# Kernel tuning notes

Measured on AMD Instinct MI355X. Metric: run time of the kernel, lower is better.

The kernel has to match this reference:

```python
import jax, jax.numpy as jnp
import numpy as np

B, S = 16, 4096
E_ENC, E_DEC, H = 1024, 1024, 512


def setup_inputs() -> dict:
    key = jax.random.key(0)
    ks = jax.random.split(key, 8)
    sc_e = 1.0 / np.sqrt(E_ENC)
    sc_d = 1.0 / np.sqrt(E_DEC)
    sc_h = 1.0 / np.sqrt(H)
    return {
        "encoder_hiddens": jax.random.normal(ks[0], (B, S, E_ENC), jnp.float32),
        "decoder_hidden": jax.random.normal(ks[1], (B, E_DEC), jnp.float32),
        "We": jax.random.uniform(ks[2], (E_ENC, H), jnp.float32, -sc_e, sc_e),
        "be": jax.random.uniform(ks[3], (H,), jnp.float32, -sc_e, sc_e),
        "Wd": jax.random.uniform(ks[4], (E_DEC, H), jnp.float32, -sc_d, sc_d),
        "bd": jax.random.uniform(ks[5], (H,), jnp.float32, -sc_d, sc_d),
        "Wo": jax.random.uniform(ks[6], (H, 1), jnp.float32, -sc_h, sc_h),
        "bo": jax.random.uniform(ks[7], (1,), jnp.float32, -sc_h, sc_h),
    }


def reference(encoder_hiddens, decoder_hidden, We, be, Wd, bd, Wo, bo):
    # Additive (Bahdanau) attention.
    # enc_proj: [B,S,H]; dec_proj: [B,1,H] broadcast over sequence.
    enc_proj = jnp.einsum("bse,eh->bsh", encoder_hiddens, We) + be
    dec_proj = jnp.einsum("bd,dh->bh", decoder_hidden, Wd) + bd
    e = jnp.tanh(enc_proj + dec_proj[:, None, :])          # [B,S,H]
    scores = jnp.einsum("bsh,h->bs", e, Wo[:, 0]) + bo[0]  # [B,S]
    attn = jax.nn.softmax(scores, axis=-1)                 # [B,S]
    context = jnp.einsum("bs,bse->be", attn, encoder_hiddens)  # [B,E_ENC]
    return context
```

## Files before the change

kernel.cpp:

```cpp
#include <hip/hip_runtime.h>
#include <hip/hip_bf16.h>
#include <math.h>

#define B_ 16
#define S_ 4096
#define E_ 1024
#define H_ 512

typedef short bf16x8 __attribute__((ext_vector_type(8)));
typedef unsigned short u16x8 __attribute__((ext_vector_type(8)));
typedef float f32x4 __attribute__((ext_vector_type(4)));

__device__ inline unsigned short f2bf(float x) {
    __hip_bfloat16 h = __float2bfloat16(x);
    return *(unsigned short*)&h;
}

__global__ __launch_bounds__(256) void we_transpose_kernel(
    const float* __restrict__ We, unsigned short* __restrict__ WeT) {
    __shared__ float sT[64][65];
    int k0 = (blockIdx.x >> 3) * 64;
    int n0 = (blockIdx.x & 7) * 64;
    int t = threadIdx.x;
#pragma unroll
    for (int p = 0; p < 16; ++p) {
        int idx = p * 256 + t;
        int k = idx >> 6, n = idx & 63;
        sT[n][k] = We[(size_t)(k0 + k) * H_ + n0 + n];
    }
    __syncthreads();
#pragma unroll
    for (int p = 0; p < 16; ++p) {
        int idx = p * 256 + t;
        int n = idx >> 6, k = idx & 63;
        WeT[(size_t)(n0 + n) * E_ + k0 + k] = f2bf(sT[n][k]);
    }
}

__global__ __launch_bounds__(256) void dp_kernel(const float* __restrict__ dec,
                                                 const float* __restrict__ Wd,
                                                 const float* __restrict__ bd,
                                                 const float* __restrict__ be,
                                                 float* __restrict__ dp) {
    int b = blockIdx.x >> 3;
    int hc = blockIdx.x & 7;
    int t = threadIdx.x;
    int h = hc * 64 + (t & 63);
    int ec = t >> 6;
    const float* dr = dec + b * E_ + ec * 256;
    const float* wp = Wd + (size_t)(ec * 256) * H_ + h;
    float acc = 0.f;
#pragma unroll 8
    for (int e = 0; e < 256; ++e) acc = fmaf(dr[e], wp[(size_t)e * H_], acc);
    __shared__ float red[4][64];
    red[ec][t & 63] = acc;
    __syncthreads();
    if (t < 64) {
        int hh = hc * 64 + t;
        dp[b * H_ + hh] = red[0][t] + red[1][t] + red[2][t] + red[3][t] + bd[hh] + be[hh];
    }
}

#define BM 128
#define BN 128
#define BK 32
#define LDA 40

__global__ __launch_bounds__(256) void scores_mfma_kernel(
    const float* __restrict__ enc, const unsigned short* __restrict__ WeT,
    const float* __restrict__ Wo, const float* __restrict__ dp,
    float* __restrict__ parts) {
    __shared__ unsigned short sA[BM * LDA];
    __shared__ unsigned short sB[BN * LDA];
    __shared__ float sRed[2][BM];

    int tid = threadIdx.x;
    int nt = blockIdx.x & 3;
    int mt = blockIdx.x >> 2;
    int m0 = mt * BM;
    int n0 = nt * BN;
    int b = m0 >> 12;
    int wave = tid >> 6, lane = tid & 63;
    int wm = wave & 1, wn = wave >> 1;
    int quad = lane >> 4, l16 = lane & 15;

    f32x4 acc[4][4];
#pragma unroll
    for (int i = 0; i < 4; ++i)
#pragma unroll
        for (int j = 0; j < 4; ++j) acc[i][j] = (f32x4)0.f;

    int am = tid >> 3;
    int ac = (tid & 7) * 4;
    const float* encP = enc + (size_t)(m0 + am) * E_ + ac;
    unsigned short* sAp = sA + am * LDA + ac;
    int bn = tid >> 1, bh = tid & 1;
    const unsigned short* wtP = WeT + (size_t)(n0 + bn) * E_ + bh * 16;
    unsigned short* sBp = sB + bn * LDA + bh * 16;

    int aBase = (wm * 64 + l16) * LDA + quad * 8;
    int bBase = (wn * 64 + l16) * LDA + quad * 8;

    for (int k0 = 0; k0 < E_; k0 += BK) {
        __syncthreads();
#pragma unroll
        for (int p = 0; p < 4; ++p) {
            float4 v = *(const float4*)(encP + (size_t)p * 32 * E_ + k0);
            ushort4 u;
            u.x = f2bf(v.x); u.y = f2bf(v.y); u.z = f2bf(v.z); u.w = f2bf(v.w);
            *(ushort4*)(sAp + p * 32 * LDA) = u;
        }
        u16x8 w0 = *(const u16x8*)(wtP + k0);
        u16x8 w1 = *(const u16x8*)(wtP + k0 + 8);
        *(u16x8*)(sBp) = w0;
        *(u16x8*)(sBp + 8) = w1;
        __syncthreads();

        bf16x8 aR[4], bR[4];
#pragma unroll
        for (int i = 0; i < 4; ++i) aR[i] = *(const bf16x8*)(sA + aBase + i * 16 * LDA);
#pragma unroll
        for (int j = 0; j < 4; ++j) bR[j] = *(const bf16x8*)(sB + bBase + j * 16 * LDA);
#pragma unroll
        for (int i = 0; i < 4; ++i)
#pragma unroll
            for (int j = 0; j < 4; ++j)
                acc[i][j] = __builtin_amdgcn_mfma_f32_16x16x32_bf16(aR[i], bR[j], acc[i][j], 0, 0, 0);
    }

    float dpv[4], wov[4];
#pragma unroll
    for (int j = 0; j < 4; ++j) {
        int h = n0 + wn * 64 + j * 16 + l16;
        dpv[j] = dp[b * H_ + h];
        wov[j] = Wo[h];
    }
    float part[4][4];
#pragma unroll
    for (int i = 0; i < 4; ++i)
#pragma unroll
        for (int r = 0; r < 4; ++r) {
            float s = 0.f;
#pragma unroll
            for (int j = 0; j < 4; ++j) {
                float x = acc[i][j][r] + dpv[j];
                float e = __expf(2.f * x);
                s += (1.f - 2.f / (e + 1.f)) * wov[j];
            }
            part[i][r] = s;
        }
#pragma unroll
    for (int i = 0; i < 4; ++i)
#pragma unroll
        for (int r = 0; r < 4; ++r) {
            float s = part[i][r];
            s += __shfl_xor(s, 1, 64);
            s += __shfl_xor(s, 2, 64);
            s += __shfl_xor(s, 4, 64);
            s += __shfl_xor(s, 8, 64);
            part[i][r] = s;
        }
    if (l16 == 0) {
#pragma unroll
        for (int i = 0; i < 4; ++i)
#pragma unroll
            for (int r = 0; r < 4; ++r)
                sRed[wn][wm * 64 + i * 16 + quad * 4 + r] = part[i][r];
    }
    __syncthreads();
    if (tid < BM) {
        float sc = sRed[0][tid] + sRed[1][tid];
        int s = (m0 & (S_ - 1)) + tid;
        parts[(size_t)(nt * B_ + b) * S_ + s] = sc;
    }
}

__global__ __launch_bounds__(256) void softmax_kernel(float* __restrict__ parts) {
    int b = blockIdx.x;
    const float* p0 = parts + (size_t)(0 * B_ + b) * S_;
    const float* p1 = parts + (size_t)(1 * B_ + b) * S_;
    const float* p2 = parts + (size_t)(2 * B_ + b) * S_;
    const float* p3 = parts + (size_t)(3 * B_ + b) * S_;
    float* row = parts + (size_t)b * S_;
    int tid = threadIdx.x;
    float v[16];
    float m = -1e30f;
#pragma unroll
    for (int i = 0; i < 16; ++i) {
        int idx = i * 256 + tid;
        v[i] = p0[idx] + p1[idx] + p2[idx] + p3[idx];
        m = fmaxf(m, v[i]);
    }
    for (int off = 32; off; off >>= 1) m = fmaxf(m, __shfl_xor(m, off, 64));
    __shared__ float redm[4];
    __shared__ float reds[4];
    if ((tid & 63) == 0) redm[tid >> 6] = m;
    __syncthreads();
    m = fmaxf(fmaxf(redm[0], redm[1]), fmaxf(redm[2], redm[3]));
    float s = 0.f;
#pragma unroll
    for (int i = 0; i < 16; ++i) {
        v[i] = __expf(v[i] - m);
        s += v[i];
    }
    for (int off = 32; off; off >>= 1) s += __shfl_xor(s, off, 64);
    if ((tid & 63) == 0) reds[tid >> 6] = s;
    __syncthreads();
    s = reds[0] + reds[1] + reds[2] + reds[3];
    float inv = 1.f / s;
#pragma unroll
    for (int i = 0; i < 16; ++i) row[i * 256 + tid] = v[i] * inv;
}

__global__ __launch_bounds__(256) void zero_kernel(float* __restrict__ out) {
    out[blockIdx.x * 256 + threadIdx.x] = 0.f;
}

__global__ __launch_bounds__(256) void ctx_kernel(const float* __restrict__ enc,
                                                  const float* __restrict__ attn,
                                                  float* __restrict__ out) {
    int b = blockIdx.x >> 5;
    int s0 = (blockIdx.x & 31) * 128;
    int tid = threadIdx.x;
    __shared__ float w[128];
    if (tid < 128) w[tid] = attn[(size_t)b * S_ + s0 + tid];
    __syncthreads();
    const float* base = enc + ((size_t)b * S_ + s0) * E_ + tid * 4;
    float4 acc = make_float4(0.f, 0.f, 0.f, 0.f);
    for (int s = 0; s < 128; ++s) {
        float4 v = *(const float4*)(base + (size_t)s * E_);
        float ws = w[s];
        acc.x = fmaf(ws, v.x, acc.x);
        acc.y = fmaf(ws, v.y, acc.y);
        acc.z = fmaf(ws, v.z, acc.z);
        acc.w = fmaf(ws, v.w, acc.w);
    }
    float* o = out + b * E_ + tid * 4;
    atomicAdd(o + 0, acc.x);
    atomicAdd(o + 1, acc.y);
    atomicAdd(o + 2, acc.z);
    atomicAdd(o + 3, acc.w);
}

extern "C" void kernel_launch(void* const* d_in, const int* in_sizes, int n_in,
                              void* d_out, int out_size, void* d_ws, size_t ws_size,
                              hipStream_t stream) {
    const float* enc = (const float*)d_in[0];
    const float* dec = (const float*)d_in[1];
    const float* We  = (const float*)d_in[2];
    const float* be  = (const float*)d_in[3];
    const float* Wd  = (const float*)d_in[4];
    const float* bd  = (const float*)d_in[5];
    const float* Wo  = (const float*)d_in[6];
    float* out = (float*)d_out;

    char* w = (char*)d_ws;
    unsigned short* WeT = (unsigned short*)w;
    float* dp = (float*)(w + (1 << 20));
    float* parts = (float*)(w + (1 << 20) + 32768);
    float* attn = parts;

    we_transpose_kernel<<<128, 256, 0, stream>>>(We, WeT);
    dp_kernel<<<B_ * 8, 256, 0, stream>>>(dec, Wd, bd, be, dp);
    scores_mfma_kernel<<<(B_ * S_ / BM) * (H_ / BN), 256, 0, stream>>>(enc, WeT, Wo, dp, parts);
    softmax_kernel<<<B_, 256, 0, stream>>>(parts);
    zero_kernel<<<(B_ * E_) / 256, 256, 0, stream>>>(out);
    ctx_kernel<<<B_ * 32, 256, 0, stream>>>(enc, attn, out);
}
```

Measured before the change: 539.6 us.

## Pre-convert encoder to bf16, use direct-to-LDS loads and deterministic context reduction

```diff
diff --git a/kernel.cpp b/kernel.cpp
--- a/kernel.cpp
+++ b/kernel.cpp
@@ -7,6 +7,11 @@
 #define E_ 1024
 #define H_ 512
 
+#define BM 128
+#define BN 128
+#define BK 64
+#define NCHUNK (E_ / BK)
+
 typedef short bf16x8 __attribute__((ext_vector_type(8)));
 typedef unsigned short u16x8 __attribute__((ext_vector_type(8)));
 typedef float f32x4 __attribute__((ext_vector_type(4)));
@@ -15,74 +20,95 @@
     __hip_bfloat16 h = __float2bfloat16(x);
     return *(unsigned short*)&h;
 }
-
-__global__ __launch_bounds__(256) void we_transpose_kernel(
-    const float* __restrict__ We, unsigned short* __restrict__ WeT) {
-    __shared__ float sT[64][65];
-    int k0 = (blockIdx.x >> 3) * 64;
-    int n0 = (blockIdx.x & 7) * 64;
-    int t = threadIdx.x;
-#pragma unroll
-    for (int p = 0; p < 16; ++p) {
-        int idx = p * 256 + t;
-        int k = idx >> 6, n = idx & 63;
-        sT[n][k] = We[(size_t)(k0 + k) * H_ + n0 + n];
-    }
-    __syncthreads();
-#pragma unroll
-    for (int p = 0; p < 16; ++p) {
-        int idx = p * 256 + t;
-        int n = idx >> 6, k = idx & 63;
-        WeT[(size_t)(n0 + n) * E_ + k0 + k] = f2bf(sT[n][k]);
-    }
-}
-
-__global__ __launch_bounds__(256) void dp_kernel(const float* __restrict__ dec,
-                                                 const float* __restrict__ Wd,
-                                                 const float* __restrict__ bd,
-                                                 const float* __restrict__ be,
-                                                 float* __restrict__ dp) {
-    int b = blockIdx.x >> 3;
-    int hc = blockIdx.x & 7;
-    int t = threadIdx.x;
-    int h = hc * 64 + (t & 63);
-    int ec = t >> 6;
-    const float* dr = dec + b * E_ + ec * 256;
-    const float* wp = Wd + (size_t)(ec * 256) * H_ + h;
-    float acc = 0.f;
+__device__ inline float bf2f(unsigned short u) {
+    unsigned int x = ((unsigned int)u) << 16;
+    float f;
+    __builtin_memcpy(&f, &x, 4);
+    return f;
+}
+__device__ __forceinline__ void gld16(const unsigned short* g, unsigned short* l) {
+    __builtin_amdgcn_global_load_lds(
+        (const __attribute__((address_space(1))) void*)g,
+        (__attribute__((address_space(3))) void*)l, 16, 0, 0);
+}
+
+__global__ __launch_bounds__(256) void prep_conv_kernel(
+    const float* __restrict__ enc, const float* __restrict__ We,
+    const float* __restrict__ dec, const float* __restrict__ Wd,
+    const float* __restrict__ bd, const float* __restrict__ be,
+    unsigned short* __restrict__ WeTcB, float* __restrict__ dp,
+    unsigned short* __restrict__ encB) {
+    __shared__ float red[4][64];
+    int bid = blockIdx.x, t = threadIdx.x;
+    if (bid < 64) {
+        int c = bid >> 2, n0t = (bid & 3) * 128;
+#pragma unroll 4
+        for (int it = 0; it < 32; ++it) {
+            int o = it * 256 + t;
+            int n_rel = o >> 6, within = o & 63;
+            int cp = within >> 3, j = within & 7;
+            int n = n0t + n_rel;
+            int k = c * 64 + ((cp ^ (n & 7)) << 3) + j;
+            WeTcB[c * 32768 + n * 64 + within] = f2bf(We[(size_t)k * H_ + n]);
+        }
+    } else if (bid < 192) {
+        int id = bid - 64;
+        int b = id >> 3, hc = id & 7;
+        int h = hc * 64 + (t & 63);
+        int ec = t >> 6;
+        const float* dr = dec + b * E_ + ec * 256;
+        const float* wp = Wd + (size_t)(ec * 256) * H_ + h;
+        float acc = 0.f;
 #pragma unroll 8
-    for (int e = 0; e < 256; ++e) acc = fmaf(dr[e], wp[(size_t)e * H_], acc);
-    __shared__ float red[4][64];
-    red[ec][t & 63] = acc;
-    __syncthreads();
-    if (t < 64) {
-        int hh = hc * 64 + t;
-        dp[b * H_ + hh] = red[0][t] + red[1][t] + red[2][t] + red[3][t] + bd[hh] + be[hh];
-    }
-}
-
-#define BM 128
-#define BN 128
-#define BK 32
-#define LDA 40
-
-__global__ __launch_bounds__(256) void scores_mfma_kernel(
-    const float* __restrict__ enc, const unsigned short* __restrict__ WeT,
+        for (int e = 0; e < 256; ++e) acc = fmaf(dr[e], wp[(size_t)e * H_], acc);
+        red[ec][t & 63] = acc;
+        __syncthreads();
+        if (t < 64) {
+            int hh = hc * 64 + t;
+            dp[b * H_ + hh] = red[0][t] + red[1][t] + red[2][t] + red[3][t] + bd[hh] + be[hh];
+        }
+    } else {
+        size_t base = ((size_t)(bid - 192) * 256 + t) * 16;
+        const float* ep = enc + base;
+        unsigned short* op = encB + base;
+        float4 v0 = *(const float4*)(ep);
+        float4 v1 = *(const float4*)(ep + 4);
+        float4 v2 = *(const float4*)(ep + 8);
+        float4 v3 = *(const float4*)(ep + 12);
+        u16x8 u0, u1;
+        u0[0] = f2bf(v0.x); u0[1] = f2bf(v0.y); u0[2] = f2bf(v0.z); u0[3] = f2bf(v0.w);
+        u0[4] = f2bf(v1.x); u0[5] = f2bf(v1.y); u0[6] = f2bf(v1.z); u0[7] = f2bf(v1.w);
+        u1[0] = f2bf(v2.x); u1[1] = f2bf(v2.y); u1[2] = f2bf(v2.z); u1[3] = f2bf(v2.w);
+        u1[4] = f2bf(v3.x); u1[5] = f2bf(v3.y); u1[6] = f2bf(v3.z); u1[7] = f2bf(v3.w);
+        *(u16x8*)(op) = u0;
+        *(u16x8*)(op + 8) = u1;
+    }
+}
+
+__global__ __launch_bounds__(256, 3) void scores_gemm_kernel(
+    const unsigned short* __restrict__ encB, const unsigned short* __restrict__ WeTcB,
     const float* __restrict__ Wo, const float* __restrict__ dp,
     float* __restrict__ parts) {
-    __shared__ unsigned short sA[BM * LDA];
-    __shared__ unsigned short sB[BN * LDA];
+    __shared__ unsigned short sA[BM * BK];
+    __shared__ unsigned short sB[BN * BK];
     __shared__ float sRed[2][BM];
 
     int tid = threadIdx.x;
+    int w = tid >> 6, l = tid & 63;
+    int l16 = l & 15, quad = l >> 4;
+    int wm = w & 1, wn = w >> 1;
     int nt = blockIdx.x & 3;
-    int mt = blockIdx.x >> 2;
-    int m0 = mt * BM;
+    size_t mt = blockIdx.x >> 2;
+    size_t m0 = mt * BM;
     int n0 = nt * BN;
-    int b = m0 >> 12;
-    int wave = tid >> 6, lane = tid & 63;
-    int wm = wave & 1, wn = wave >> 1;
-    int quad = lane >> 4, l16 = lane & 15;
+    int b = (int)(m0 >> 12);
+
+    int lrow = l >> 3, lcp = l & 7;
+    int qa = lcp ^ (lrow & 7);
+    const unsigned short* gA = encB + (m0 + w * 8 + lrow) * E_ + qa * 8;
+    const unsigned short* gB = WeTcB + (size_t)n0 * BK + (w * 8) * BK + l * 8;
+    unsigned short* sAb = sA + (w * 8) * BK;
+    unsigned short* sBb = sB + (w * 8) * BK;
 
     f32x4 acc[4][4];
 #pragma unroll
@@ -90,52 +116,45 @@
 #pragma unroll
         for (int j = 0; j < 4; ++j) acc[i][j] = (f32x4)0.f;
 
-    int am = tid >> 3;
-    int ac = (tid & 7) * 4;
-    const float* encP = enc + (size_t)(m0 + am) * E_ + ac;
-    unsigned short* sAp = sA + am * LDA + ac;
-    int bn = tid >> 1, bh = tid & 1;
-    const unsigned short* wtP = WeT + (size_t)(n0 + bn) * E_ + bh * 16;
-    unsigned short* sBp = sB + bn * LDA + bh * 16;
-
-    int aBase = (wm * 64 + l16) * LDA + quad * 8;
-    int bBase = (wn * 64 + l16) * LDA + quad * 8;
-
-    for (int k0 = 0; k0 < E_; k0 += BK) {
+    int arow = (wm * 64 + l16) * BK;
+    int brow = (wn * 64 + l16) * BK;
+    int sw = l16 & 7;
+
+    for (int c = 0; c < NCHUNK; ++c) {
         __syncthreads();
-#pragma unroll
-        for (int p = 0; p < 4; ++p) {
-            float4 v = *(const float4*)(encP + (size_t)p * 32 * E_ + k0);
-            ushort4 u;
-            u.x = f2bf(v.x); u.y = f2bf(v.y); u.z = f2bf(v.z); u.w = f2bf(v.w);
-            *(ushort4*)(sAp + p * 32 * LDA) = u;
-        }
-        u16x8 w0 = *(const u16x8*)(wtP + k0);
-        u16x8 w1 = *(const u16x8*)(wtP + k0 + 8);
-        *(u16x8*)(sBp) = w0;
-        *(u16x8*)(sBp + 8) = w1;
+        int k0 = c * BK;
+#pragma unroll
+        for (int i = 0; i < 4; ++i) {
+            gld16(gA + (size_t)i * 32 * E_ + k0, sAb + i * 32 * BK);
+            gld16(gB + (size_t)c * (H_ * BK) + i * 32 * BK, sBb + i * 32 * BK);
+        }
         __syncthreads();
-
-        bf16x8 aR[4], bR[4];
-#pragma unroll
-        for (int i = 0; i < 4; ++i) aR[i] = *(const bf16x8*)(sA + aBase + i * 16 * LDA);
-#pragma unroll
-        for (int j = 0; j < 4; ++j) bR[j] = *(const bf16x8*)(sB + bBase + j * 16 * LDA);
-#pragma unroll
-        for (int i = 0; i < 4; ++i)
+#pragma unroll
+        for (int half = 0; half < 2; ++half) {
+            int koff = (((half * 4 + quad) ^ sw) << 3);
+            bf16x8 aR[4], bR[4];
+#pragma unroll
+            for (int i = 0; i < 4; ++i)
+                aR[i] = *(const bf16x8*)(sA + arow + i * 16 * BK + koff);
 #pragma unroll
             for (int j = 0; j < 4; ++j)
-                acc[i][j] = __builtin_amdgcn_mfma_f32_16x16x32_bf16(aR[i], bR[j], acc[i][j], 0, 0, 0);
+                bR[j] = *(const bf16x8*)(sB + brow + j * 16 * BK + koff);
+#pragma unroll
+            for (int i = 0; i < 4; ++i)
+#pragma unroll
+                for (int j = 0; j < 4; ++j)
+                    acc[i][j] = __builtin_amdgcn_mfma_f32_16x16x32_bf16(aR[i], bR[j], acc[i][j], 0, 0, 0);
+        }
     }
 
     float dpv[4], wov[4];
+    const float* dpb = dp + b * H_;
 #pragma unroll
     for (int j = 0; j < 4; ++j) {
         int h = n0 + wn * 64 + j * 16 + l16;
-        dpv[j] = dp[b * H_ + h];
+        dpv[j] = dpb[h];
         wov[j] = Wo[h];
     }
-    float part[4][4];
 #pragma unroll
     for (int i = 0; i < 4; ++i)
 #pragma unroll
@@ -147,49 +166,37 @@
                 float e = __expf(2.f * x);
                 s += (1.f - 2.f / (e + 1.f)) * wov[j];
             }
-            part[i][r] = s;
-        }
-#pragma unroll
-    for (int i = 0; i < 4; ++i)
-#pragma unroll
-        for (int r = 0; r < 4; ++r) {
-            float s = part[i][r];
             s += __shfl_xor(s, 1, 64);
             s += __shfl_xor(s, 2, 64);
             s += __shfl_xor(s, 4, 64);
             s += __shfl_xor(s, 8, 64);
-            part[i][r] = s;
-        }
-    if (l16 == 0) {
-#pragma unroll
-        for (int i = 0; i < 4; ++i)
-#pragma unroll
-            for (int r = 0; r < 4; ++r)
-                sRed[wn][wm * 64 + i * 16 + quad * 4 + r] = part[i][r];
-    }
+            if (l16 == 0) sRed[wn][wm * 64 + i * 16 + quad * 4 + r] = s;
+        }
     __syncthreads();
     if (tid < BM) {
-        float sc = sRed[0][tid] + sRed[1][tid];
-        int s = (m0 & (S_ - 1)) + tid;
-        parts[(size_t)(nt * B_ + b) * S_ + s] = sc;
+        int s_in = (int)(m0 & (S_ - 1)) + tid;
+        parts[(size_t)(nt * B_ + b) * S_ + s_in] = sRed[0][tid] + sRed[1][tid];
     }
 }
 
 __global__ __launch_bounds__(256) void softmax_kernel(float* __restrict__ parts) {
-    int b = blockIdx.x;
-    const float* p0 = parts + (size_t)(0 * B_ + b) * S_;
-    const float* p1 = parts + (size_t)(1 * B_ + b) * S_;
-    const float* p2 = parts + (size_t)(2 * B_ + b) * S_;
-    const float* p3 = parts + (size_t)(3 * B_ + b) * S_;
-    float* row = parts + (size_t)b * S_;
-    int tid = threadIdx.x;
-    float v[16];
+    int b = blockIdx.x, tid = threadIdx.x;
+    const float4* p0 = (const float4*)(parts + (size_t)(0 * B_ + b) * S_);
+    const float4* p1 = (const float4*)(parts + (size_t)(1 * B_ + b) * S_);
+    const float4* p2 = (const float4*)(parts + (size_t)(2 * B_ + b) * S_);
+    const float4* p3 = (const float4*)(parts + (size_t)(3 * B_ + b) * S_);
+    float4* row = (float4*)(parts + (size_t)b * S_);
+    float4 v[4];
     float m = -1e30f;
 #pragma unroll
-    for (int i = 0; i < 16; ++i) {
+    for (int i = 0; i < 4; ++i) {
         int idx = i * 256 + tid;
-        v[i] = p0[idx] + p1[idx] + p2[idx] + p3[idx];
-        m = fmaxf(m, v[i]);
+        float4 a0 = p0[idx], a1 = p1[idx], a2 = p2[idx], a3 = p3[idx];
+        v[i].x = a0.x + a1.x + a2.x + a3.x;
+        v[i].y = a0.y + a1.y + a2.y + a3.y;
+        v[i].z = a0.z + a1.z + a2.z + a3.z;
+        v[i].w = a0.w + a1.w + a2.w + a3.w;
+        m = fmaxf(m, fmaxf(fmaxf(v[i].x, v[i].y), fmaxf(v[i].z, v[i].w)));
     }
     for (int off = 32; off; off >>= 1) m = fmaxf(m, __shfl_xor(m, off, 64));
     __shared__ float redm[4];
@@ -199,9 +206,10 @@
     m = fmaxf(fmaxf(redm[0], redm[1]), fmaxf(redm[2], redm[3]));
     float s = 0.f;
 #pragma unroll
-    for (int i = 0; i < 16; ++i) {
-        v[i] = __expf(v[i] - m);
-        s += v[i];
+    for (int i = 0; i < 4; ++i) {
+        v[i].x = __expf(v[i].x - m); v[i].y = __expf(v[i].y - m);
+        v[i].z = __expf(v[i].z - m); v[i].w = __expf(v[i].w - m);
+        s += (v[i].x + v[i].y) + (v[i].z + v[i].w);
     }
     for (int off = 32; off; off >>= 1) s += __shfl_xor(s, off, 64);
     if ((tid & 63) == 0) reds[tid >> 6] = s;
@@ -209,37 +217,59 @@
     s = reds[0] + reds[1] + reds[2] + reds[3];
     float inv = 1.f / s;
 #pragma unroll
-    for (int i = 0; i < 16; ++i) row[i * 256 + tid] = v[i] * inv;
-}
-
-__global__ __launch_bounds__(256) void zero_kernel(float* __restrict__ out) {
-    out[blockIdx.x * 256 + threadIdx.x] = 0.f;
-}
-
-__global__ __launch_bounds__(256) void ctx_kernel(const float* __restrict__ enc,
-                                                  const float* __restrict__ attn,
-                                                  float* __restrict__ out) {
+    for (int i = 0; i < 4; ++i) {
+        int idx = i * 256 + tid;
+        row[idx] = make_float4(v[i].x * inv, v[i].y * inv, v[i].z * inv, v[i].w * inv);
+    }
+}
+
+__global__ __launch_bounds__(256) void ctx_partial_bf16(
+    const unsigned short* __restrict__ encB, const float* __restrict__ attn,
+    float* __restrict__ part) {
     int b = blockIdx.x >> 5;
-    int s0 = (blockIdx.x & 31) * 128;
+    int c = blockIdx.x & 31;
+    int s0 = c * 128;
     int tid = threadIdx.x;
     __shared__ float w[128];
     if (tid < 128) w[tid] = attn[(size_t)b * S_ + s0 + tid];
     __syncthreads();
-    const float* base = enc + ((size_t)b * S_ + s0) * E_ + tid * 4;
-    float4 acc = make_float4(0.f, 0.f, 0.f, 0.f);
-    for (int s = 0; s < 128; ++s) {
-        float4 v = *(const float4*)(base + (size_t)s * E_);
-        float ws = w[s];
-        acc.x = fmaf(ws, v.x, acc.x);
-        acc.y = fmaf(ws, v.y, acc.y);
-        acc.z = fmaf(ws, v.z, acc.z);
-        acc.w = fmaf(ws, v.w, acc.w);
-    }
-    float* o = out + b * E_ + tid * 4;
-    atomicAdd(o + 0, acc.x);
-    atomicAdd(o + 1, acc.y);
-    atomicAdd(o + 2, acc.z);
-    atomicAdd(o + 3, acc.w);
+    int e8 = (tid & 127) * 8;
+    int sh = tid >> 7;
+    const unsigned short* base = encB + ((size_t)b * S_ + s0 + sh * 64) * E_ + e8;
+    const float* wp = w + sh * 64;
+    float acc[8];
+#pragma unroll
+    for (int t = 0; t < 8; ++t) acc[t] = 0.f;
+    for (int s = 0; s < 64; s += 8) {
+        u16x8 v[8];
+#pragma unroll
+        for (int u = 0; u < 8; ++u) v[u] = *(const u16x8*)(base + (size_t)(s + u) * E_);
+#pragma unroll
+        for (int u = 0; u < 8; ++u) {
+            float ws = wp[s + u];
+#pragma unroll
+            for (int t = 0; t < 8; ++t) acc[t] = fmaf(ws, bf2f(v[u][t]), acc[t]);
+        }
+    }
+    float* po = part + ((size_t)(b * 64 + c * 2 + sh)) * E_ + e8;
+    *(float4*)(po) = make_float4(acc[0], acc[1], acc[2], acc[3]);
+    *(float4*)(po + 4) = make_float4(acc[4], acc[5], acc[6], acc[7]);
+}
+
+__global__ __launch_bounds__(256) void ctx_reduce(const float* __restrict__ part,
+                                                  float* __restrict__ out, int nch) {
+    int idx = blockIdx.x * 256 + threadIdx.x;
+    int b = idx >> 10;
+    int e = idx & 1023;
+    const float* p = part + (size_t)b * nch * E_ + e;
+    float s0 = 0.f, s1 = 0.f, s2 = 0.f, s3 = 0.f;
+    for (int c = 0; c < nch; c += 4) {
+        s0 += p[(size_t)(c + 0) * E_];
+        s1 += p[(size_t)(c + 1) * E_];
+        s2 += p[(size_t)(c + 2) * E_];
+        s3 += p[(size_t)(c + 3) * E_];
+    }
+    out[idx] = (s0 + s1) + (s2 + s3);
 }
 
 extern "C" void kernel_launch(void* const* d_in, const int* in_sizes, int n_in,
@@ -254,16 +284,19 @@
     const float* Wo  = (const float*)d_in[6];
     float* out = (float*)d_out;
 
-    char* w = (char*)d_ws;
-    unsigned short* WeT = (unsigned short*)w;
-    float* dp = (float*)(w + (1 << 20));
-    float* parts = (float*)(w + (1 << 20) + 32768);
+    char* wsp = (char*)d_ws;
+    unsigned short* WeTcB = (unsigned short*)wsp;
+    float* dp = (float*)(wsp + (1 << 20));
+    float* parts = (float*)(wsp + (1 << 20) + (64 << 10));
+    float* part = (float*)(wsp + (4 << 20));
+    unsigned short* encB = (unsigned short*)(wsp + (8 << 20));
     float* attn = parts;
 
-    we_transpose_kernel<<<128, 256, 0, stream>>>(We, WeT);
-    dp_kernel<<<B_ * 8, 256, 0, stream>>>(dec, Wd, bd, be, dp);
-    scores_mfma_kernel<<<(B_ * S_ / BM) * (H_ / BN), 256, 0, stream>>>(enc, WeT, Wo, dp, parts);
+    prep_conv_kernel<<<192 + 16384, 256, 0, stream>>>(enc, We, dec, Wd, bd, be,
+                                                      WeTcB, dp, encB);
+    scores_gemm_kernel<<<(B_ * S_ / BM) * (H_ / BN), 256, 0, stream>>>(
+        encB, WeTcB, Wo, dp, parts);
     softmax_kernel<<<B_, 256, 0, stream>>>(parts);
-    zero_kernel<<<(B_ * E_) / 256, 256, 0, stream>>>(out);
-    ctx_kernel<<<B_ * 32, 256, 0, stream>>>(enc, attn, out);
-}
+    ctx_partial_bf16<<<B_ * 32, 256, 0, stream>>>(encB, attn, part);
+    ctx_reduce<<<B_ * E_ / 256, 256, 0, stream>>>(part, out, 64);
+}
```

Result: faster. 495.9 us (-8.1%).
